# Optimization experiments

Hardware: AMD Instinct MI355X
Metric: run time of the kernel (lower is better)

## Reference

```python
import jax, jax.numpy as jnp
import numpy as np

B, S, D = 32, 512, 1024
H, DH = 16, 64
EPS, TEMP = 1e-7, 0.1
P_LOGIT_INIT = float(np.log(0.2) - np.log(0.8))  # init_min == init_max == 0.2


def setup_inputs() -> dict:
    key = jax.random.key(0)
    ks = jax.random.split(key, 10)
    x = jax.random.normal(ks[0], (B, S, D), dtype=jnp.float32)
    lengths_x = jax.random.randint(ks[1], (B,), 0, S - 1)
    lengths_x = lengths_x.at[0].set(S - 1)  # ensure max(lengths)+1 == S, as torch code assumes
    Wq = jax.random.normal(ks[2], (D, H * DH), dtype=jnp.float32) * 0.02
    Wk = jax.random.normal(ks[3], (D, H * DH), dtype=jnp.float32) * 0.02
    Wv = jax.random.normal(ks[4], (D, H * DH), dtype=jnp.float32) * 0.02
    Wo = jax.random.normal(ks[5], (H * DH, D), dtype=jnp.float32) * 0.02
    p_logits = jnp.full((4,), P_LOGIT_INIT, dtype=jnp.float32)  # q, k, v, o
    noise_q = jax.random.uniform(ks[6], (B, S, D), dtype=jnp.float32)
    noise_k = jax.random.uniform(ks[7], (B, S, D), dtype=jnp.float32)
    noise_v = jax.random.uniform(ks[8], (B, S, D), dtype=jnp.float32)
    noise_o = jax.random.uniform(ks[9], (B, S, H * DH), dtype=jnp.float32)
    return {"x": x, "lengths_x": lengths_x, "Wq": Wq, "Wk": Wk, "Wv": Wv,
            "Wo": Wo, "p_logits": p_logits, "noise_q": noise_q,
            "noise_k": noise_k, "noise_v": noise_v, "noise_o": noise_o}


def _concrete_dropout(x, p_logit, u):
    p = jax.nn.sigmoid(p_logit)
    drop_prob = jax.nn.sigmoid(
        (jnp.log(p + EPS) - jnp.log(1.0 - p + EPS)
         + jnp.log(u + EPS) - jnp.log(1.0 - u + EPS)) / TEMP)
    return x * (1.0 - drop_prob) / (1.0 - p)


def reference(x, lengths_x, Wq, Wk, Wv, Wo, p_logits, noise_q, noise_k, noise_v, noise_o):
    b, s, _ = x.shape
    q = (_concrete_dropout(x, p_logits[0], noise_q) @ Wq).reshape(b, s, H, DH)
    k = (_concrete_dropout(x, p_logits[1], noise_k) @ Wk).reshape(b, s, H, DH)
    v = (_concrete_dropout(x, p_logits[2], noise_v) @ Wv).reshape(b, s, H, DH)
    e = jnp.einsum('bxhd,byhd->bhxy', q, k) / np.sqrt(DH).astype(np.float32)
    # mask[b, i, j] = 1 iff i <= lengths[b] and j <= lengths[b]
    valid = jnp.arange(s)[None, :] <= lengths_x[:, None]          # [B, S]
    mask = (valid[:, :, None] & valid[:, None, :])[:, None, :, :]  # [B, 1, S, S]
    e = jnp.where(mask, e, jnp.float32(-1e10))
    alpha = jax.nn.softmax(e, axis=-1)                             # [B, H, S, S]
    out = jnp.einsum('bhxy,byhd->bxhd', alpha, v).reshape(b, s, H * DH)
    out = _concrete_dropout(out, p_logits[3], noise_o) @ Wo
    return jax.nn.relu(out), alpha
```

## Files before the change

kernel.cpp:

```cpp
#include <hip/hip_runtime.h>

constexpr int B_ = 32, S_ = 512, D_ = 1024, H_ = 16, DH_ = 64, HD_ = 1024;
constexpr int M_ = B_ * S_;
constexpr float EPS_ = 1e-7f;
constexpr float INV_TEMP_ = 10.0f;

typedef __attribute__((ext_vector_type(8))) short bf16x8;
typedef __attribute__((ext_vector_type(4))) short bf16x4;
typedef __attribute__((ext_vector_type(4))) float f32x4;
typedef __attribute__((ext_vector_type(8))) unsigned short us8;

__device__ __forceinline__ float sigm(float x) { return 1.0f / (1.0f + __expf(-x)); }

__device__ __forceinline__ unsigned short f2bf(float f) {
    unsigned u = __float_as_uint(f);
    unsigned r = (u + 0x7FFFu + ((u >> 16) & 1u)) >> 16;
    return (unsigned short)r;
}

#define GLL16(gp, lp) __builtin_amdgcn_global_load_lds( \
    (const __attribute__((address_space(1))) unsigned int*)(gp), \
    (__attribute__((address_space(3))) unsigned int*)(lp), 16, 0, 0)

__device__ __forceinline__ bf16x8 ldsfrag64(const unsigned short* base, int row, int k) {
    int slot = ((k >> 3) ^ (row & 7)) << 3;
    return *(const bf16x8*)(base + row * 64 + slot);
}

__global__ __launch_bounds__(256)
void cd_cast3_kernel(const float* __restrict__ x,
                     const float* __restrict__ nq, const float* __restrict__ nk,
                     const float* __restrict__ nv, const float* __restrict__ pl,
                     unsigned short* __restrict__ aq, unsigned short* __restrict__ ak,
                     unsigned short* __restrict__ av)
{
    size_t i0 = ((size_t)blockIdx.x * 256 + threadIdx.x) * 8;

    float c0[3], inv1mp[3];
#pragma unroll
    for (int j = 0; j < 3; ++j) {
        float p = sigm(pl[j]);
        c0[j] = __logf(p + EPS_) - __logf(1.0f - p + EPS_);
        inv1mp[j] = 1.0f / (1.0f - p);
    }

    float4 x0 = *(const float4*)(x + i0);
    float4 x1 = *(const float4*)(x + i0 + 4);
    float xv[8] = {x0.x, x0.y, x0.z, x0.w, x1.x, x1.y, x1.z, x1.w};

    const float* ns[3] = {nq, nk, nv};
    unsigned short* os[3] = {aq, ak, av};
#pragma unroll
    for (int j = 0; j < 3; ++j) {
        float4 u0 = *(const float4*)(ns[j] + i0);
        float4 u1 = *(const float4*)(ns[j] + i0 + 4);
        float uv[8] = {u0.x, u0.y, u0.z, u0.w, u1.x, u1.y, u1.z, u1.w};
        ushort out[8];
#pragma unroll
        for (int t = 0; t < 8; ++t) {
            float lt = (c0[j] + __logf(uv[t] + EPS_) - __logf(1.0f - uv[t] + EPS_)) * INV_TEMP_;
            float dpr = sigm(lt);
            out[t] = f2bf(xv[t] * (1.0f - dpr) * inv1mp[j]);
        }
        *(us8*)(os[j] + i0) = *(us8*)out;
    }
}

__global__ __launch_bounds__(256)
void wcast_t4_kernel(const float* __restrict__ W0, const float* __restrict__ W1,
                     const float* __restrict__ W2, const float* __restrict__ W3,
                     unsigned short* __restrict__ T0, unsigned short* __restrict__ T1,
                     unsigned short* __restrict__ T2, unsigned short* __restrict__ T3)
{
    __shared__ unsigned short t[64][72];
    int z = blockIdx.z;
    const float* W = (z & 2) ? ((z & 1) ? W3 : W2) : ((z & 1) ? W1 : W0);
    unsigned short* WT = (z & 2) ? ((z & 1) ? T3 : T2) : ((z & 1) ? T1 : T0);
    int kb = blockIdx.y * 64;
    int nb = blockIdx.x * 64;
    int tid = threadIdx.x;
#pragma unroll
    for (int i = 0; i < 4; ++i) {
        int idx = tid + i * 256;
        int r = idx >> 4, c4 = idx & 15;
        float4 v = *(const float4*)(W + (size_t)(kb + r) * 1024 + nb + c4 * 4);
        t[c4 * 4 + 0][r] = f2bf(v.x);
        t[c4 * 4 + 1][r] = f2bf(v.y);
        t[c4 * 4 + 2][r] = f2bf(v.z);
        t[c4 * 4 + 3][r] = f2bf(v.w);
    }
    __syncthreads();
#pragma unroll
    for (int i = 0; i < 4; ++i) {
        int idx = tid + i * 256;
        int r = idx >> 4, c4 = idx & 15;
        ushort4 o;
        o.x = t[r][c4 * 4 + 0];
        o.y = t[r][c4 * 4 + 1];
        o.z = t[r][c4 * 4 + 2];
        o.w = t[r][c4 * 4 + 3];
        *(ushort4*)(WT + (size_t)(nb + r) * 1024 + kb + c4 * 4) = o;
    }
}

__global__ __launch_bounds__(256, 3)
void gemm_qkv_kernel(const unsigned short* __restrict__ A,
                     const unsigned short* __restrict__ BT,
                     unsigned short* __restrict__ qkb,
                     unsigned short* __restrict__ vT)
{
    const int zo = blockIdx.y;
    A  += (size_t)zo * M_ * HD_;
    BT += (size_t)zo * (1024 * 1024);

    __shared__ unsigned short LDSU[8704];
    unsigned short* As = LDSU;
    unsigned short* Bs = LDSU + 4096;

    int flat = blockIdx.x;
    int swz = (flat & 7) * 128 + (flat >> 3);
    int ntile = swz & 7, mtile = swz >> 3;
    int m0 = mtile * 128, n0 = ntile * 128;

    int tid = threadIdx.x;
    int w = tid >> 6, lane = tid & 63;
    int wm = w >> 1, wn = w & 1;

    f32x4 acc[4][4];
#pragma unroll
    for (int m = 0; m < 4; ++m)
#pragma unroll
        for (int n = 0; n < 4; ++n) acc[m][n] = (f32x4){0.f, 0.f, 0.f, 0.f};

    const unsigned short* Ag = A + (size_t)(m0 + w * 32 + (lane >> 2)) * 1024 + (lane & 3) * 8;
    const unsigned short* Bg = BT + (size_t)(n0 + w * 32 + (lane >> 2)) * 1024 + (lane & 3) * 8;
    unsigned short* AsW = As + (w * 32) * 32;
    unsigned short* BsW = Bs + (w * 32) * 32;

    const int arow = wm * 64 + (lane & 15);
    const int brow = wn * 64 + (lane & 15);
    const int koff = (lane >> 4) * 8;

    for (int k0 = 0; k0 < 1024; k0 += 32) {
        __syncthreads();
        GLL16(Ag + k0,             AsW);
        GLL16(Ag + k0 + 16 * 1024, AsW + 16 * 32);
        GLL16(Bg + k0,             BsW);
        GLL16(Bg + k0 + 16 * 1024, BsW + 16 * 32);
        __syncthreads();

        bf16x8 afr[4], bfr[4];
#pragma unroll
        for (int m = 0; m < 4; ++m)
            afr[m] = *(const bf16x8*)&As[(arow + m * 16) * 32 + koff];
#pragma unroll
        for (int n = 0; n < 4; ++n)
            bfr[n] = *(const bf16x8*)&Bs[(brow + n * 16) * 32 + koff];
#pragma unroll
        for (int m = 0; m < 4; ++m)
#pragma unroll
            for (int n = 0; n < 4; ++n)
                acc[m][n] = __builtin_amdgcn_mfma_f32_16x16x32_bf16(afr[m], bfr[n], acc[m][n], 0, 0, 0);
    }

    const int cr = (lane >> 4) * 4, cc = lane & 15;
    __syncthreads();

    if (zo < 2) {
        unsigned short* Cb = qkb + (size_t)zo * M_ * HD_;
        for (int n = 0; n < 4; ++n) {
#pragma unroll
            for (int m = 0; m < 4; ++m)
#pragma unroll
                for (int j = 0; j < 4; ++j)
                    LDSU[(wm * 64 + m * 16 + cr + j) * 68 + wn * 16 + cc] = f2bf(acc[m][n][j]);
            __syncthreads();
#pragma unroll
            for (int t = 0; t < 2; ++t) {
                int fl = tid + t * 256;
                int row = fl >> 2, p = fl & 3;
                us8 vv = *(const us8*)&LDSU[row * 68 + p * 8];
                int colg = n0 + (p >> 1) * 64 + n * 16 + (p & 1) * 8;
                *(us8*)(Cb + (size_t)(m0 + row) * 1024 + colg) = vv;
            }
            __syncthreads();
        }
    } else {
        int b = m0 >> 9, y0 = m0 & 511, h0 = n0 >> 6;
        for (int n = 0; n < 4; ++n) {
#pragma unroll
            for (int m = 0; m < 4; ++m)
#pragma unroll
                for (int j = 0; j < 4; ++j)
                    LDSU[(wn * 16 + cc) * 132 + wm * 64 + m * 16 + cr + j] = f2bf(acc[m][n][j]);
            __syncthreads();
#pragma unroll
            for (int t = 0; t < 2; ++t) {
                int fl = tid + t * 256;
                int cl = fl >> 4, yp = fl & 15;
                us8 vv = *(const us8*)&LDSU[cl * 132 + yp * 8];
                int h = h0 + (cl >> 4), d = n * 16 + (cl & 15);
                *(us8*)(vT + ((size_t)((b * 16 + h) * 64 + d)) * 512 + y0 + yp * 8) = vv;
            }
            __syncthreads();
        }
    }
}

__global__ __launch_bounds__(256, 3)
void gemm_o_kernel(const unsigned short* __restrict__ A,
                   const unsigned short* __restrict__ BT,
                   float* __restrict__ C)
{
    __shared__ unsigned short As[128 * 32];
    __shared__ unsigned short Bs[128 * 32];

    int flat = blockIdx.x;
    int swz = (flat & 7) * 128 + (flat >> 3);
    int ntile = swz & 7, mtile = swz >> 3;
    int m0 = mtile * 128, n0 = ntile * 128;

    int tid = threadIdx.x;
    int w = tid >> 6, lane = tid & 63;
    int wm = w >> 1, wn = w & 1;

    f32x4 acc[4][4];
#pragma unroll
    for (int m = 0; m < 4; ++m)
#pragma unroll
        for (int n = 0; n < 4; ++n) acc[m][n] = (f32x4){0.f, 0.f, 0.f, 0.f};

    const unsigned short* Ag = A + (size_t)(m0 + w * 32 + (lane >> 2)) * 1024 + (lane & 3) * 8;
    const unsigned short* Bg = BT + (size_t)(n0 + w * 32 + (lane >> 2)) * 1024 + (lane & 3) * 8;
    unsigned short* AsW = As + (w * 32) * 32;
    unsigned short* BsW = Bs + (w * 32) * 32;

    const int arow = wm * 64 + (lane & 15);
    const int brow = wn * 64 + (lane & 15);
    const int koff = (lane >> 4) * 8;

    for (int k0 = 0; k0 < 1024; k0 += 32) {
        __syncthreads();
        GLL16(Ag + k0,             AsW);
        GLL16(Ag + k0 + 16 * 1024, AsW + 16 * 32);
        GLL16(Bg + k0,             BsW);
        GLL16(Bg + k0 + 16 * 1024, BsW + 16 * 32);
        __syncthreads();

        bf16x8 afr[4], bfr[4];
#pragma unroll
        for (int m = 0; m < 4; ++m)
            afr[m] = *(const bf16x8*)&As[(arow + m * 16) * 32 + koff];
#pragma unroll
        for (int n = 0; n < 4; ++n)
            bfr[n] = *(const bf16x8*)&Bs[(brow + n * 16) * 32 + koff];
#pragma unroll
        for (int m = 0; m < 4; ++m)
#pragma unroll
            for (int n = 0; n < 4; ++n)
                acc[m][n] = __builtin_amdgcn_mfma_f32_16x16x32_bf16(afr[m], bfr[n], acc[m][n], 0, 0, 0);
    }

    int cr = (lane >> 4) * 4, cc = lane & 15;
#pragma unroll
    for (int m = 0; m < 4; ++m)
#pragma unroll
        for (int n = 0; n < 4; ++n)
#pragma unroll
            for (int j = 0; j < 4; ++j) {
                int row = m0 + wm * 64 + m * 16 + cr + j;
                int col = n0 + wn * 64 + n * 16 + cc;
                C[(size_t)row * 1024 + col] = fmaxf(acc[m][n][j], 0.f);
            }
}

__global__ __launch_bounds__(512, 2)
void fused_attn2_kernel(const unsigned short* __restrict__ qb,
                        const unsigned short* __restrict__ kb,
                        const unsigned short* __restrict__ vT,
                        const float* __restrict__ no,
                        const float* __restrict__ pl,
                        const int* __restrict__ lengths,
                        float* __restrict__ alpha,
                        unsigned short* __restrict__ Ao)
{
    const int bh = blockIdx.x;
    const int b = bh >> 4, h = bh & 15;
    const int tid = threadIdx.x;
    const int w = tid >> 6, lane = tid & 63;
    const int g = lane >> 4, li = lane & 15;
    const int len = lengths[b];

    __shared__ unsigned short Kall[512 * 64];
    __shared__ unsigned short Vall[8 * 64 * 64];
    __shared__ unsigned short Olb[128 * 72];

    const int sr = lane >> 3;
    const int sc = ((lane & 7) ^ sr) * 8;

    {
        const size_t kbase = ((size_t)(b * 512 + w * 64)) * 1024 + h * 64;
        const size_t vbase = ((size_t)bh * 64) * 512;
#pragma unroll
        for (int c = 0; c < 8; ++c) {
            GLL16(kb + kbase + (size_t)(c * 8 + sr) * 1024 + sc, Kall + w * 4096 + c * 512);
            GLL16(vT + vbase + (size_t)(c * 8 + sr) * 512 + w * 64 + sc, Vall + w * 4096 + c * 512);
        }
    }
    __syncthreads();

    const float po = sigm(pl[3]);
    const float c0o = __logf(po + EPS_) - __logf(1.0f - po + EPS_);
    const float inv1mpo = 1.0f / (1.0f - po);

    for (int qt = 0; qt < 4; ++qt) {
        const int xg = qt * 128 + w * 16 + li;

        const unsigned short* qp = qb + ((size_t)(b * 512 + xg)) * 1024 + h * 64 + g * 8;
        bf16x8 qf0 = *(const bf16x8*)qp;
        bf16x8 qf1 = *(const bf16x8*)(qp + 32);

        f32x4 acc[32];
#pragma unroll
        for (int f = 0; f < 32; ++f) acc[f] = (f32x4){0.f, 0.f, 0.f, 0.f};

#pragma unroll
        for (int f = 0; f < 32; ++f) {
            bf16x8 kf0 = ldsfrag64(Kall, f * 16 + li, g * 8);
            bf16x8 kf1 = ldsfrag64(Kall, f * 16 + li, g * 8 + 32);
            acc[f] = __builtin_amdgcn_mfma_f32_16x16x32_bf16(kf0, qf0, acc[f], 0, 0, 0);
            acc[f] = __builtin_amdgcn_mfma_f32_16x16x32_bf16(kf1, qf1, acc[f], 0, 0, 0);
        }

        const bool vx = (xg <= len);
        float mx = -3.4e38f;
#pragma unroll
        for (int f = 0; f < 32; ++f)
#pragma unroll
            for (int r = 0; r < 4; ++r) {
                int y = f * 16 + g * 4 + r;
                float s = (vx && (y <= len)) ? acc[f][r] * 0.125f : -1e10f;
                acc[f][r] = s;
                mx = fmaxf(mx, s);
            }
        mx = fmaxf(mx, __shfl_xor(mx, 16));
        mx = fmaxf(mx, __shfl_xor(mx, 32));
        float sum = 0.f;
#pragma unroll
        for (int f = 0; f < 32; ++f)
#pragma unroll
            for (int r = 0; r < 4; ++r) {
                float e = __expf(acc[f][r] - mx);
                acc[f][r] = e;
                sum += e;
            }
        sum += __shfl_xor(sum, 16);
        sum += __shfl_xor(sum, 32);
        const float inv = 1.0f / sum;

        float* arow = alpha + ((size_t)bh * 512 + xg) * 512;
#pragma unroll
        for (int f = 0; f < 32; ++f) {
            f32x4 av = acc[f];
            av[0] *= inv; av[1] *= inv; av[2] *= inv; av[3] *= inv;
            acc[f] = av;
            __builtin_nontemporal_store(av, (f32x4*)(arow + f * 16 + g * 4));
        }

        f32x4 acco[4];
#pragma unroll
        for (int cf = 0; cf < 4; ++cf) acco[cf] = (f32x4){0.f, 0.f, 0.f, 0.f};

#pragma unroll
        for (int yt = 0; yt < 8; ++yt) {
            const unsigned short* Vc = Vall + yt * 4096;
#pragma unroll
            for (int w2 = 0; w2 < 2; ++w2) {
                int f0 = yt * 4 + w2 * 2;
                bf16x8 pf;
#pragma unroll
                for (int r = 0; r < 4; ++r) {
                    pf[r]     = (short)f2bf(acc[f0][r]);
                    pf[4 + r] = (short)f2bf(acc[f0 + 1][r]);
                }
#pragma unroll
                for (int cf = 0; cf < 4; ++cf) {
                    int d = cf * 16 + li;
                    int s0 = w2 * 8 + g;
                    int s1 = s0 + 4;
                    int p0 = (((s0 >> 1) ^ (d & 7)) << 3) + ((s0 & 1) << 2);
                    int p1 = (((s1 >> 1) ^ (d & 7)) << 3) + ((s1 & 1) << 2);
                    bf16x4 lo = *(const bf16x4*)(Vc + d * 64 + p0);
                    bf16x4 hi = *(const bf16x4*)(Vc + d * 64 + p1);
                    bf16x8 vf;
#pragma unroll
                    for (int e = 0; e < 4; ++e) { vf[e] = lo[e]; vf[4 + e] = hi[e]; }
                    acco[cf] = __builtin_amdgcn_mfma_f32_16x16x32_bf16(pf, vf, acco[cf], 0, 0, 0);
                }
            }
        }

#pragma unroll
        for (int cf = 0; cf < 4; ++cf)
#pragma unroll
            for (int r = 0; r < 4; ++r)
                Olb[(w * 16 + g * 4 + r) * 72 + cf * 16 + li] = f2bf(acco[cf][r]);
        __syncthreads();

#pragma unroll
        for (int i = 0; i < 2; ++i) {
            int idx = tid + i * 512;
            int xr = idx >> 3, d0 = (idx & 7) * 8;
            int xglob = qt * 128 + xr;
            const float* nop = no + ((size_t)(b * 512 + xglob)) * 1024 + h * 64 + d0;
            float4 n0 = *(const float4*)nop;
            float4 n1 = *(const float4*)(nop + 4);
            float nn[8] = {n0.x, n0.y, n0.z, n0.w, n1.x, n1.y, n1.z, n1.w};
            us8 ov = *(const us8*)&Olb[xr * 72 + d0];
            ushort o[8];
#pragma unroll
            for (int e = 0; e < 8; ++e) {
                float val = __uint_as_float(((unsigned)ov[e]) << 16);
                float lt = (c0o + __logf(nn[e] + EPS_) - __logf(1.0f - nn[e] + EPS_)) * INV_TEMP_;
                o[e] = f2bf(val * (1.0f - sigm(lt)) * inv1mpo);
            }
            *(us8*)(Ao + ((size_t)(b * 512 + xglob)) * 1024 + h * 64 + d0) = *(us8*)o;
        }
        __syncthreads();
    }
}

extern "C" void kernel_launch(void* const* d_in, const int* in_sizes, int n_in,
                              void* d_out, int out_size, void* d_ws, size_t ws_size,
                              hipStream_t stream)
{
    const float* x       = (const float*)d_in[0];
    const int*   lengths = (const int*)d_in[1];
    const float* Wq      = (const float*)d_in[2];
    const float* Wk      = (const float*)d_in[3];
    const float* Wv      = (const float*)d_in[4];
    const float* Wo      = (const float*)d_in[5];
    const float* pl      = (const float*)d_in[6];
    const float* nq      = (const float*)d_in[7];
    const float* nk      = (const float*)d_in[8];
    const float* nv      = (const float*)d_in[9];
    const float* no      = (const float*)d_in[10];

    float* outp   = (float*)d_out;
    float* alphaF = outp + (size_t)M_ * D_;

    const size_t chunk = (size_t)M_ * HD_;
    unsigned short* qb  = (unsigned short*)d_ws;
    unsigned short* kb  = qb + chunk;
    unsigned short* vT  = kb + chunk;
    unsigned short* Ao  = vT + chunk;
    unsigned short* WTo = Ao + chunk;

    unsigned short* WTq = (unsigned short*)(alphaF);
    unsigned short* Aq  = (unsigned short*)(alphaF + 1572864);
    unsigned short* WTk = WTq + (size_t)1024 * 1024;
    unsigned short* WTv = WTk + (size_t)1024 * 1024;

    dim3 blk(256);
    wcast_t4_kernel<<<dim3(16, 16, 4), blk, 0, stream>>>(Wq, Wk, Wv, Wo, WTq, WTk, WTv, WTo);

    cd_cast3_kernel<<<8192, blk, 0, stream>>>(x, nq, nk, nv, pl, Aq, Aq + chunk, Aq + 2 * chunk);

    gemm_qkv_kernel<<<dim3(1024, 3), blk, 0, stream>>>(Aq, WTq, qb, vT);

    fused_attn2_kernel<<<512, 512, 0, stream>>>(qb, kb, vT, no, pl, lengths, alphaF, Ao);

    gemm_o_kernel<<<1024, blk, 0, stream>>>(Ao, WTo, outp);
}
```

Measured before the change: 482.1 us.

## Split attention key range across two wave halves with cross-wave softmax merge

The attention kernel now runs 1024 threads per block. The two halves of the waves each handle 256 of the 512 keys for the same query rows. Per-half max and sum are exchanged through shared memory to form the exact softmax, and the partial PV outputs are reduced through LDS before the output dropout. Blocks are also remapped so that consecutive block IDs are spread across batch/head. This halves per-wave register accumulators and raises wave-level parallelism, at the cost of more barriers and the LDS reduction traffic. Launch bounds of (1024,4) may be unattainable given the LDS footprint.

```diff
diff --git a/kernel.cpp b/kernel.cpp
--- a/kernel.cpp
+++ b/kernel.cpp
@@ -274,8 +274,8 @@
             }
 }
 
-__global__ __launch_bounds__(512, 2)
-void fused_attn2_kernel(const unsigned short* __restrict__ qb,
+__global__ __launch_bounds__(1024, 4)
+void fused_attn3_kernel(const unsigned short* __restrict__ qb,
                         const unsigned short* __restrict__ kb,
                         const unsigned short* __restrict__ vT,
                         const float* __restrict__ no,
@@ -284,28 +284,37 @@
                         float* __restrict__ alpha,
                         unsigned short* __restrict__ Ao)
 {
-    const int bh = blockIdx.x;
+    const int flat = blockIdx.x;
+    const int bh = (flat & 7) * 64 + (flat >> 3);
     const int b = bh >> 4, h = bh & 15;
     const int tid = threadIdx.x;
     const int w = tid >> 6, lane = tid & 63;
     const int g = lane >> 4, li = lane & 15;
+    const int xw = w & 7;
+    const int half = w >> 3;
     const int len = lengths[b];
 
     __shared__ unsigned short Kall[512 * 64];
-    __shared__ unsigned short Vall[8 * 64 * 64];
-    __shared__ unsigned short Olb[128 * 72];
+    __shared__ unsigned short Vall[512 * 64];
+    __shared__ unsigned short Olb[128 * 64];
+    __shared__ float msX[128][2][2];
+
+    float* OlbF = (float*)Olb;
 
     const int sr = lane >> 3;
     const int sc = ((lane & 7) ^ sr) * 8;
 
     {
-        const size_t kbase = ((size_t)(b * 512 + w * 64)) * 1024 + h * 64;
-        const size_t vbase = ((size_t)bh * 64) * 512;
-#pragma unroll
-        for (int c = 0; c < 8; ++c) {
-            GLL16(kb + kbase + (size_t)(c * 8 + sr) * 1024 + sc, Kall + w * 4096 + c * 512);
-            GLL16(vT + vbase + (size_t)(c * 8 + sr) * 512 + w * 64 + sc, Vall + w * 4096 + c * 512);
-        }
+        const size_t kbase = ((size_t)(b * 512 + w * 32)) * 1024 + h * 64;
+#pragma unroll
+        for (int c = 0; c < 4; ++c)
+            GLL16(kb + kbase + (size_t)(c * 8 + sr) * 1024 + sc, Kall + (w * 32 + c * 8) * 64);
+        const int yt = w >> 1, dbase = (w & 1) * 32;
+        const size_t vbase = ((size_t)bh * 64 + dbase) * 512;
+#pragma unroll
+        for (int c = 0; c < 4; ++c)
+            GLL16(vT + vbase + (size_t)(c * 8 + sr) * 512 + yt * 64 + sc,
+                  Vall + yt * 4096 + (dbase + c * 8) * 64);
     }
     __syncthreads();
 
@@ -314,55 +323,64 @@
     const float inv1mpo = 1.0f / (1.0f - po);
 
     for (int qt = 0; qt < 4; ++qt) {
-        const int xg = qt * 128 + w * 16 + li;
+        const int xg = qt * 128 + xw * 16 + li;
 
         const unsigned short* qp = qb + ((size_t)(b * 512 + xg)) * 1024 + h * 64 + g * 8;
         bf16x8 qf0 = *(const bf16x8*)qp;
         bf16x8 qf1 = *(const bf16x8*)(qp + 32);
 
-        f32x4 acc[32];
-#pragma unroll
-        for (int f = 0; f < 32; ++f) acc[f] = (f32x4){0.f, 0.f, 0.f, 0.f};
-
-#pragma unroll
-        for (int f = 0; f < 32; ++f) {
-            bf16x8 kf0 = ldsfrag64(Kall, f * 16 + li, g * 8);
-            bf16x8 kf1 = ldsfrag64(Kall, f * 16 + li, g * 8 + 32);
+        f32x4 acc[16];
+#pragma unroll
+        for (int f = 0; f < 16; ++f) acc[f] = (f32x4){0.f, 0.f, 0.f, 0.f};
+
+#pragma unroll
+        for (int f = 0; f < 16; ++f) {
+            int krow = half * 256 + f * 16 + li;
+            bf16x8 kf0 = ldsfrag64(Kall, krow, g * 8);
+            bf16x8 kf1 = ldsfrag64(Kall, krow, g * 8 + 32);
             acc[f] = __builtin_amdgcn_mfma_f32_16x16x32_bf16(kf0, qf0, acc[f], 0, 0, 0);
             acc[f] = __builtin_amdgcn_mfma_f32_16x16x32_bf16(kf1, qf1, acc[f], 0, 0, 0);
         }
 
         const bool vx = (xg <= len);
-        float mx = -3.4e38f;
-#pragma unroll
-        for (int f = 0; f < 32; ++f)
+        float mh = -3.4e38f;
+#pragma unroll
+        for (int f = 0; f < 16; ++f)
 #pragma unroll
             for (int r = 0; r < 4; ++r) {
-                int y = f * 16 + g * 4 + r;
+                int y = half * 256 + f * 16 + g * 4 + r;
                 float s = (vx && (y <= len)) ? acc[f][r] * 0.125f : -1e10f;
                 acc[f][r] = s;
-                mx = fmaxf(mx, s);
+                mh = fmaxf(mh, s);
             }
-        mx = fmaxf(mx, __shfl_xor(mx, 16));
-        mx = fmaxf(mx, __shfl_xor(mx, 32));
-        float sum = 0.f;
-#pragma unroll
-        for (int f = 0; f < 32; ++f)
+        mh = fmaxf(mh, __shfl_xor(mh, 16));
+        mh = fmaxf(mh, __shfl_xor(mh, 32));
+        float sh = 0.f;
+#pragma unroll
+        for (int f = 0; f < 16; ++f)
 #pragma unroll
             for (int r = 0; r < 4; ++r) {
-                float e = __expf(acc[f][r] - mx);
+                float e = __expf(acc[f][r] - mh);
                 acc[f][r] = e;
-                sum += e;
+                sh += e;
             }
-        sum += __shfl_xor(sum, 16);
-        sum += __shfl_xor(sum, 32);
-        const float inv = 1.0f / sum;
-
-        float* arow = alpha + ((size_t)bh * 512 + xg) * 512;
-#pragma unroll
-        for (int f = 0; f < 32; ++f) {
+        sh += __shfl_xor(sh, 16);
+        sh += __shfl_xor(sh, 32);
+
+        const int xl = xw * 16 + li;
+        if (g == 0) { msX[xl][half][0] = mh; msX[xl][half][1] = sh; }
+        __syncthreads();
+        float mo = msX[xl][half ^ 1][0];
+        float so = msX[xl][half ^ 1][1];
+        float M = fmaxf(mh, mo);
+        float S = sh * __expf(mh - M) + so * __expf(mo - M);
+        const float csc = __expf(mh - M) / S;
+
+        float* arow = alpha + ((size_t)bh * 512 + xg) * 512 + half * 256;
+#pragma unroll
+        for (int f = 0; f < 16; ++f) {
             f32x4 av = acc[f];
-            av[0] *= inv; av[1] *= inv; av[2] *= inv; av[3] *= inv;
+            av[0] *= csc; av[1] *= csc; av[2] *= csc; av[3] *= csc;
             acc[f] = av;
             __builtin_nontemporal_store(av, (f32x4*)(arow + f * 16 + g * 4));
         }
@@ -372,11 +390,11 @@
         for (int cf = 0; cf < 4; ++cf) acco[cf] = (f32x4){0.f, 0.f, 0.f, 0.f};
 
 #pragma unroll
-        for (int yt = 0; yt < 8; ++yt) {
-            const unsigned short* Vc = Vall + yt * 4096;
+        for (int yth = 0; yth < 4; ++yth) {
+            const unsigned short* Vc = Vall + (half * 4 + yth) * 4096;
 #pragma unroll
             for (int w2 = 0; w2 < 2; ++w2) {
-                int f0 = yt * 4 + w2 * 2;
+                int f0 = yth * 4 + w2 * 2;
                 bf16x8 pf;
 #pragma unroll
                 for (int r = 0; r < 4; ++r) {
@@ -400,31 +418,54 @@
             }
         }
 
-#pragma unroll
-        for (int cf = 0; cf < 4; ++cf)
-#pragma unroll
-            for (int r = 0; r < 4; ++r)
-                Olb[(w * 16 + g * 4 + r) * 72 + cf * 16 + li] = f2bf(acco[cf][r]);
-        __syncthreads();
-
-#pragma unroll
-        for (int i = 0; i < 2; ++i) {
-            int idx = tid + i * 512;
-            int xr = idx >> 3, d0 = (idx & 7) * 8;
-            int xglob = qt * 128 + xr;
-            const float* nop = no + ((size_t)(b * 512 + xglob)) * 1024 + h * 64 + d0;
-            float4 n0 = *(const float4*)nop;
-            float4 n1 = *(const float4*)(nop + 4);
-            float nn[8] = {n0.x, n0.y, n0.z, n0.w, n1.x, n1.y, n1.z, n1.w};
-            us8 ov = *(const us8*)&Olb[xr * 72 + d0];
-            ushort o[8];
-#pragma unroll
-            for (int e = 0; e < 8; ++e) {
-                float val = __uint_as_float(((unsigned)ov[e]) << 16);
-                float lt = (c0o + __logf(nn[e] + EPS_) - __logf(1.0f - nn[e] + EPS_)) * INV_TEMP_;
-                o[e] = f2bf(val * (1.0f - sigm(lt)) * inv1mpo);
-            }
-            *(us8*)(Ao + ((size_t)(b * 512 + xglob)) * 1024 + h * 64 + d0) = *(us8*)o;
+        __syncthreads();
+        if (half == 1) {
+#pragma unroll
+            for (int cf = 0; cf < 2; ++cf)
+#pragma unroll
+                for (int r = 0; r < 4; ++r)
+                    OlbF[(xw * 16 + g * 4 + r) * 32 + cf * 16 + li] = acco[cf][r];
+        }
+        __syncthreads();
+        if (half == 0) {
+#pragma unroll
+            for (int cf = 0; cf < 2; ++cf)
+#pragma unroll
+                for (int r = 0; r < 4; ++r)
+                    acco[cf][r] += OlbF[(xw * 16 + g * 4 + r) * 32 + cf * 16 + li];
+        }
+        __syncthreads();
+        if (half == 1) {
+#pragma unroll
+            for (int cf = 2; cf < 4; ++cf)
+#pragma unroll
+                for (int r = 0; r < 4; ++r)
+                    OlbF[(xw * 16 + g * 4 + r) * 32 + (cf - 2) * 16 + li] = acco[cf][r];
+        }
+        __syncthreads();
+        if (half == 0) {
+#pragma unroll
+            for (int cf = 2; cf < 4; ++cf)
+#pragma unroll
+                for (int r = 0; r < 4; ++r)
+                    acco[cf][r] += OlbF[(xw * 16 + g * 4 + r) * 32 + (cf - 2) * 16 + li];
+#pragma unroll
+            for (int cf = 0; cf < 4; ++cf)
+#pragma unroll
+                for (int r = 0; r < 4; ++r) {
+                    int row = qt * 128 + xw * 16 + g * 4 + r;
+                    int d = cf * 16 + li;
+                    float nn = no[((size_t)(b * 512 + row)) * 1024 + h * 64 + d];
+                    float lt = (c0o + __logf(nn + EPS_) - __logf(1.0f - nn + EPS_)) * INV_TEMP_;
+                    float val = acco[cf][r] * (1.0f - sigm(lt)) * inv1mpo;
+                    Olb[(xw * 16 + g * 4 + r) * 64 + d] = f2bf(val);
+                }
+        }
+        __syncthreads();
+        {
+            int xr = tid >> 3, d0 = (tid & 7) * 8;
+            us8 ov = *(const us8*)&Olb[xr * 64 + d0];
+            *(us8*)(Ao + ((size_t)(b * 512 + qt * 128 + xr)) * 1024 + h * 64 + d0) = ov;
         }
         __syncthreads();
     }
@@ -468,7 +509,7 @@
 
     gemm_qkv_kernel<<<dim3(1024, 3), blk, 0, stream>>>(Aq, WTq, qb, vT);
 
-    fused_attn2_kernel<<<512, 512, 0, stream>>>(qb, kb, vT, no, pl, lengths, alphaF, Ao);
+    fused_attn3_kernel<<<512, 1024, 0, stream>>>(qb, kb, vT, no, pl, lengths, alphaF, Ao);
 
     gemm_o_kernel<<<1024, blk, 0, stream>>>(Ao, WTo, outp);
 }
```

Measured after the change: 591.3 us. 1.23x slower.
